# Performance work log

Hardware: AMD Instinct MI355X
Metric: run time of the kernel (lower is better)

The kernel has to match this reference:

```python
import jax, jax.numpy as jnp
import numpy as np

B, T, D, H = 8, 4096, 512, 64

def setup_inputs() -> dict:
    key = jax.random.key(0)
    ks = jax.random.split(key, 6)
    s = 0.02  # small init scale so exp(K), exp(wbias) stay numerically tame
    return {
        "x": jax.random.normal(ks[0], (B, T, D), dtype=jnp.float32),
        "wq": jax.random.normal(ks[1], (H, D), dtype=jnp.float32) * s,
        "bq": jnp.zeros((H,), dtype=jnp.float32),
        "wk": jax.random.normal(ks[2], (H, D), dtype=jnp.float32) * s,
        "bk": jnp.zeros((H,), dtype=jnp.float32),
        "wv": jax.random.normal(ks[3], (H, D), dtype=jnp.float32) * s,
        "bv": jnp.zeros((H,), dtype=jnp.float32),
        "wp": jax.random.normal(ks[4], (D, H), dtype=jnp.float32) * s,
        "bp": jnp.zeros((D,), dtype=jnp.float32),
        "wbias": jax.random.normal(ks[5], (T, T), dtype=jnp.float32) * s,
    }

def reference(x, wq, bq, wk, bk, wv, bv, wp, bp, wbias):
    # Q, K, V projections: [B, T, H]
    Q = jnp.einsum('btd,hd->bth', x, wq) + bq
    K = jnp.einsum('btd,hd->bth', x, wk) + bk
    V = jnp.einsum('btd,hd->bth', x, wv) + bv
    ew = jnp.exp(wbias)              # [T, T], computed once
    eK = jnp.exp(K)                  # [B, T, H]
    num = jnp.einsum('ts,bsh->bth', ew, eK * V)
    den = jnp.einsum('ts,bsh->bth', ew, eK)
    Yt = jax.nn.sigmoid(Q) * (num / den)
    # output projection back to dim: [B, T, D]
    return jnp.einsum('bth,dh->btd', Yt, wp) + bp
```

## Files before the change

kernel.cpp:

```cpp
#include <hip/hip_runtime.h>
#include <math.h>

typedef _Float16 f16;
typedef __attribute__((ext_vector_type(8))) _Float16 f16x8;
typedef __attribute__((ext_vector_type(4))) _Float16 f16x4;
typedef __attribute__((ext_vector_type(4))) float f32x4;
typedef __attribute__((ext_vector_type(16))) float f32x16;

#define MFMA16(a, b, c) __builtin_amdgcn_mfma_f32_16x16x32_f16((a), (b), (c), 0, 0, 0)
#define MFMA32(a, b, c) __builtin_amdgcn_mfma_f32_32x32x16_f16((a), (b), (c), 0, 0, 0)

__device__ __forceinline__ void gld16(const f16* g, f16* l) {
  __builtin_amdgcn_global_load_lds(
      (const __attribute__((address_space(1))) unsigned int*)g,
      (__attribute__((address_space(3))) unsigned int*)l, 16, 0, 0);
}

__device__ __forceinline__ f16x8 pack8(const float* src) {
  float4 f0 = *(const float4*)src;
  float4 f1 = *(const float4*)(src + 4);
  f16x8 v;
  v[0] = (f16)f0.x; v[1] = (f16)f0.y; v[2] = (f16)f0.z; v[3] = (f16)f0.w;
  v[4] = (f16)f1.x; v[5] = (f16)f1.y; v[6] = (f16)f1.z; v[7] = (f16)f1.w;
  return v;
}

__global__ __launch_bounds__(256) void prep_ewpw(const float* __restrict__ wb,
                                                 f16* __restrict__ ew,
                                                 const float* __restrict__ wq,
                                                 const float* __restrict__ wk,
                                                 const float* __restrict__ wv,
                                                 const float* __restrict__ wp,
                                                 f16* __restrict__ wqkvb,
                                                 f16* __restrict__ wpf) {
  const size_t stride = (size_t)gridDim.x * 256;
  const size_t total = (size_t)4096 * 4096 / 4;
  for (size_t i = (size_t)blockIdx.x * 256 + threadIdx.x; i < total; i += stride) {
    float4 f = ((const float4*)wb)[i];
    f16x4 o;
    o.x = (f16)expf(f.x); o.y = (f16)expf(f.y);
    o.z = (f16)expf(f.z); o.w = (f16)expf(f.w);
    ((f16x4*)ew)[i] = o;
  }
  if (blockIdx.x < 128) {
    int i = blockIdx.x * 256 + threadIdx.x;
    wqkvb[i] = (f16)wk[i];
    wqkvb[32768 + i] = (f16)wv[i];
    wqkvb[65536 + i] = (f16)wq[i];
  }
  if (blockIdx.x == 128) {
    const int tid = threadIdx.x;
#pragma unroll
    for (int u = 0; u < 16; ++u) {
      int d = u * 256 + tid;
      int dcb = d >> 8, c = (d >> 6) & 3, l = d & 63;
      const float* src = wp + (size_t)(dcb * 32 + (l & 31)) * 64 + c * 16 + (l >> 5) * 8;
      f16x8 o;
#pragma unroll
      for (int e = 0; e < 8; ++e) o[e] = (f16)src[e];
      *(f16x8*)(wpf + ((size_t)d << 3)) = o;
    }
  }
}

__global__ __launch_bounds__(256) void k1_qkv(const float* __restrict__ x,
                                              const f16* __restrict__ wqkvb,
                                              const float* __restrict__ bq,
                                              const float* __restrict__ bk,
                                              const float* __restrict__ bv,
                                              f16* __restrict__ sigQ,
                                              f16* __restrict__ XT) {
  __shared__ alignas(16) f16 sW[192 * 64];
  __shared__ alignas(16) f16 sX[64 * 64];
  const int tid = threadIdx.x;
  const int wave = tid >> 6, lane = tid & 63;
  const int m0 = blockIdx.x * 64;
  const int l15 = lane & 15;

  f32x4 accQ[4], accK[4], accV[4];
#pragma unroll
  for (int j = 0; j < 4; ++j) {
    accQ[j] = (f32x4){0.f, 0.f, 0.f, 0.f};
    accK[j] = (f32x4){0.f, 0.f, 0.f, 0.f};
    accV[j] = (f32x4){0.f, 0.f, 0.f, 0.f};
  }

  const int sc8 = tid & 7;
  const int wr8 = (tid >> 3) & 7;
  const int wcol = (sc8 ^ wr8) * 8;

  for (int ks = 0; ks < 512; ks += 64) {
#pragma unroll
    for (int q = 0; q < 6; ++q) {
      int r = q * 32 + (tid >> 3);
      gld16(wqkvb + (size_t)r * 512 + ks + wcol, &sW[r * 64 + sc8 * 8]);
    }
#pragma unroll
    for (int u = 0; u < 2; ++u) {
      int un = tid + u * 256;
      int r = un >> 3, c8 = un & 7;
      *(f16x8*)&sX[r * 64 + ((c8 ^ (r & 7)) * 8)] =
          pack8(x + (size_t)(m0 + r) * 512 + ks + c8 * 8);
    }
    __syncthreads();
#pragma unroll
    for (int kk = 0; kk < 2; ++kk) {
      const int c = kk * 4 + (lane >> 4);
      const int rK = wave * 16 + l15;
      const int rV = 64 + rK;
      f16x8 aK = *(const f16x8*)&sW[rK * 64 + ((c ^ (rK & 7)) * 8)];
      f16x8 aV = *(const f16x8*)&sW[rV * 64 + ((c ^ (rV & 7)) * 8)];
      f16x8 aQ = *(const f16x8*)&sX[rK * 64 + ((c ^ (rK & 7)) * 8)];
#pragma unroll
      for (int j = 0; j < 4; ++j) {
        const int rX = j * 16 + l15;
        const int rWq = 128 + j * 16 + l15;
        f16x8 bx = *(const f16x8*)&sX[rX * 64 + ((c ^ (rX & 7)) * 8)];
        f16x8 bw = *(const f16x8*)&sW[rWq * 64 + ((c ^ (rWq & 7)) * 8)];
        accK[j] = MFMA16(aK, bx, accK[j]);
        accV[j] = MFMA16(aV, bx, accV[j]);
        accQ[j] = MFMA16(aQ, bw, accQ[j]);
      }
    }
    __syncthreads();
  }
  const int b = m0 >> 12, t0 = m0 & 4095;
#pragma unroll
  for (int j = 0; j < 4; ++j) {
    const int h = j * 16 + l15;
    const float bqv = bq[h];
#pragma unroll
    for (int r = 0; r < 4; ++r) {
      const int m = m0 + wave * 16 + (lane >> 4) * 4 + r;
      const float v = accQ[j][r] + bqv;
      sigQ[(size_t)m * 64 + h] = (f16)(1.f / (1.f + expf(-v)));
    }
  }
#pragma unroll
  for (int r = 0; r < 4; ++r) {
    const int h = wave * 16 + (lane >> 4) * 4 + r;
    const float bkv = bk[h], bvv = bv[h];
    const size_t rowKV = (size_t)(b * 128 + h) * 4096;
    const size_t rowK = (size_t)(b * 128 + 64 + h) * 4096;
#pragma unroll
    for (int j = 0; j < 4; ++j) {
      const int t = t0 + j * 16 + l15;
      const float ek = expf(accK[j][r] + bkv);
      const float ev = accV[j][r] + bvv;
      XT[rowKV + t] = (f16)(ek * ev);
      XT[rowK + t] = (f16)ek;
    }
  }
}

__global__ __launch_bounds__(256) void k2_main(const f16* __restrict__ A,
                                               const f16* __restrict__ Bm,
                                               f16* __restrict__ P) {
  __shared__ alignas(16) f16 smem[2][2][8192];
  const int tid = threadIdx.x;
  const int w = tid >> 6, lane = tid & 63;
  const int wr = w >> 1, wc = w & 1;
  const int bid = blockIdx.x;
  const int x = bid & 7, y = bid >> 3;
  const int mt = x * 4 + (y >> 4);
  const int rem = y & 15;
  const int b = rem >> 1, kh = rem & 1;
  const int m0 = mt * 128;
  const size_t k0 = (size_t)kh * 2048;
  const f16* Ab = A + (size_t)m0 * 4096 + k0;
  const f16* Bb = Bm + (size_t)(b * 128) * 4096 + k0;

  int sRow[4], sCol[4];
#pragma unroll
  for (int u = 0; u < 4; ++u) {
    int d = u * 256 + tid;
    int p = d >> 4, c16 = d & 15;
    int oc = c16 ^ (p & 15);
    sRow[u] = p + 64 * (oc >> 3);
    sCol[u] = (oc & 7) * 8;
  }

  f32x16 accN[2], accD[2];
#pragma unroll
  for (int i = 0; i < 2; ++i)
#pragma unroll
    for (int r = 0; r < 16; ++r) { accN[i][r] = 0.f; accD[i][r] = 0.f; }

#define SB0 __builtin_amdgcn_sched_barrier(0)
#define K2_STAGE(buf, ks)                                                       \
  do {                                                                          \
    _Pragma("unroll") for (int u = 0; u < 4; ++u)                               \
        gld16(Ab + (size_t)sRow[u] * 4096 + (ks) + sCol[u],                     \
              &smem[buf][0][(u * 256 + tid) * 8]);                              \
    _Pragma("unroll") for (int u = 0; u < 4; ++u)                               \
        gld16(Bb + (size_t)sRow[u] * 4096 + (ks) + sCol[u],                     \
              &smem[buf][1][(u * 256 + tid) * 8]);                              \
  } while (0)

  K2_STAGE(0, 0);
  K2_STAGE(1, 64);
  asm volatile("s_waitcnt vmcnt(8)" ::: "memory");
  SB0;
  __builtin_amdgcn_s_barrier();
  SB0;

  const int l31 = lane & 31, l15 = lane & 15, lhi = lane >> 5;
  const int nk = 32;
  for (int t = 0; t < nk; ++t) {
    const int cur = t & 1;
    const f16* pA = smem[cur][0];
    const f16* pB = smem[cur][1];
    __builtin_amdgcn_s_setprio(1);
#pragma unroll
    for (int ks4 = 0; ks4 < 4; ++ks4) {
      const int kcc = ks4 * 2 + lhi;
      f16x8 a0 = *(const f16x8*)&pA[(l31)*128 + (((wr * 8 + kcc) ^ l15) * 8)];
      f16x8 a1 = *(const f16x8*)&pA[(32 + l31) * 128 + (((wr * 8 + kcc) ^ l15) * 8)];
      f16x8 bn = *(const f16x8*)&pB[(wc * 32 + l31) * 128 + ((kcc ^ l15) * 8)];
      f16x8 bd = *(const f16x8*)&pB[(wc * 32 + l31) * 128 + (((8 + kcc) ^ l15) * 8)];
      accN[0] = MFMA32(a0, bn, accN[0]);
      accD[0] = MFMA32(a0, bd, accD[0]);
      accN[1] = MFMA32(a1, bn, accN[1]);
      accD[1] = MFMA32(a1, bd, accD[1]);
    }
    __builtin_amdgcn_s_setprio(0);
    asm volatile("s_waitcnt lgkmcnt(0)" ::: "memory");
    SB0;
    __builtin_amdgcn_s_barrier();
    SB0;
    if (t + 2 < nk) {
      K2_STAGE(cur, (t + 2) * 64);
      asm volatile("s_waitcnt vmcnt(8)" ::: "memory");
    } else {
      asm volatile("s_waitcnt vmcnt(0)" ::: "memory");
    }
    SB0;
    __builtin_amdgcn_s_barrier();
    SB0;
  }
#undef K2_STAGE
#undef SB0

  f16* Pp = P + (size_t)kh * 4194304 + (size_t)(mt * 8 + b) * 16384;
#pragma unroll
  for (int i = 0; i < 2; ++i) {
#pragma unroll
    for (int r = 0; r < 16; ++r) {
      const int crow = wr * 64 + i * 32 + (r & 3) + 8 * (r >> 2) + 4 * lhi;
      Pp[crow * 128 + wc * 32 + l31] = (f16)accN[i][r];
      Pp[crow * 128 + 64 + wc * 32 + l31] = (f16)accD[i][r];
    }
  }
}

__global__ __launch_bounds__(256) void k2_red(const f16* __restrict__ P,
                                              const f16* __restrict__ sigQ,
                                              const f16* __restrict__ wpf,
                                              const float* __restrict__ bp,
                                              float* __restrict__ out) {
  __shared__ alignas(16) f16 sYt[128 * 72];
  const int tid = threadIdx.x;
  const int rid = blockIdx.x;
  const int mt = (rid & 7) * 4 + ((rid >> 3) & 3);
  const int b = rid >> 5;
  const int m0 = mt * 128;
  const f16* P0 = P + (size_t)(mt * 8 + b) * 16384;
  const f16* P1 = P0 + 4194304;

#pragma unroll
  for (int u = 0; u < 4; ++u) {
    const int e = u * 256 + tid;
    const int row = e >> 3, c = e & 7;
    f16x8 n0 = *(const f16x8*)(P0 + row * 128 + c * 8);
    f16x8 n1 = *(const f16x8*)(P1 + row * 128 + c * 8);
    f16x8 d0 = *(const f16x8*)(P0 + row * 128 + 64 + c * 8);
    f16x8 d1 = *(const f16x8*)(P1 + row * 128 + 64 + c * 8);
    f16x8 sq = *(const f16x8*)(sigQ + ((size_t)b * 4096 + m0 + row) * 64 + c * 8);
    f16x8 yv;
#pragma unroll
    for (int e8 = 0; e8 < 8; ++e8) {
      const float num = (float)n0[e8] + (float)n1[e8];
      const float den = (float)d0[e8] + (float)d1[e8];
      yv[e8] = (f16)((float)sq[e8] * num / den);
    }
    *(f16x8*)&sYt[row * 72 + c * 8] = yv;
  }
  __syncthreads();

  const int w = tid >> 6, lane = tid & 63;
  const int l31 = lane & 31, lhi = lane >> 5;
  f16x8 ay[4];
#pragma unroll
  for (int c = 0; c < 4; ++c)
    ay[c] = *(const f16x8*)&sYt[(w * 32 + l31) * 72 + c * 16 + lhi * 8];
#pragma unroll
  for (int cbo = 0; cbo < 16; ++cbo) {
    f32x16 oacc;
#pragma unroll
    for (int r = 0; r < 16; ++r) oacc[r] = 0.f;
#pragma unroll
    for (int c = 0; c < 4; ++c) {
      f16x8 bw = *(const f16x8*)(wpf + (((size_t)cbo * 4 + c) * 64 + lane) * 8);
      oacc = MFMA32(ay[c], bw, oacc);
    }
    const int od = cbo * 32 + l31;
    const float bpv = bp[od];
#pragma unroll
    for (int r = 0; r < 16; ++r) {
      const int orow = w * 32 + (r & 3) + 8 * (r >> 2) + 4 * lhi;
      out[((size_t)(b * 4096 + m0 + orow)) * 512 + od] = oacc[r] + bpv;
    }
  }
}

extern "C" void kernel_launch(void* const* d_in, const int* in_sizes, int n_in,
                              void* d_out, int out_size, void* d_ws, size_t ws_size,
                              hipStream_t stream) {
  const float* x = (const float*)d_in[0];
  const float* wq = (const float*)d_in[1];
  const float* bq = (const float*)d_in[2];
  const float* wk = (const float*)d_in[3];
  const float* bk = (const float*)d_in[4];
  const float* wv = (const float*)d_in[5];
  const float* bv = (const float*)d_in[6];
  const float* wp = (const float*)d_in[7];
  const float* bp = (const float*)d_in[8];
  const float* wbias = (const float*)d_in[9];
  float* out = (float*)d_out;

  char* ws = (char*)d_ws;
  f16* ew = (f16*)(ws);
  f16* XT = (f16*)(ws + 33554432);
  f16* sigQ = (f16*)(ws + 41943040);
  f16* P = (f16*)(ws + 46137344);
  f16* wqkvb = (f16*)(ws + 62914560);
  f16* wpf = (f16*)(ws + 63111168);

  prep_ewpw<<<4096, 256, 0, stream>>>(wbias, ew, wq, wk, wv, wp, wqkvb, wpf);
  k1_qkv<<<512, 256, 0, stream>>>(x, wqkvb, bq, bk, bv, sigQ, XT);
  k2_main<<<512, 256, 0, stream>>>(ew, XT, P);
  k2_red<<<256, 256, 0, stream>>>(P, sigQ, wpf, bp, out);
}
```

Baseline: 108.6 us.

## Fuse prep and QKV projection into one kernel; re-split reduction kernel

Merges the exp(wbias) prep kernel and the QKV projection kernel into a single launch. Blocks 0-511 do the projection and the remaining 2048 blocks do the exp conversion and the wp repack, so the two independent jobs run concurrently and one launch disappears. The projection now loads the fp32 weights and converts them to f16 inline instead of using a pre-converted f16 copy. That repeats the conversion work in every block and drops the async global-to-LDS load path. The reduction/output-projection kernel now uses 512 threads per block over half-row tiles with twice as many blocks, and each wave handles two output column blocks with two row groups.

Result: faster. 100.4 us (-7.5%).

```diff
diff --git a/kernel.cpp b/kernel.cpp
--- a/kernel.cpp
+++ b/kernel.cpp
@@ -25,54 +25,49 @@
   return v;
 }
 
-__global__ __launch_bounds__(256) void prep_ewpw(const float* __restrict__ wb,
-                                                 f16* __restrict__ ew,
-                                                 const float* __restrict__ wq,
-                                                 const float* __restrict__ wk,
-                                                 const float* __restrict__ wv,
-                                                 const float* __restrict__ wp,
-                                                 f16* __restrict__ wqkvb,
-                                                 f16* __restrict__ wpf) {
-  const size_t stride = (size_t)gridDim.x * 256;
-  const size_t total = (size_t)4096 * 4096 / 4;
-  for (size_t i = (size_t)blockIdx.x * 256 + threadIdx.x; i < total; i += stride) {
-    float4 f = ((const float4*)wb)[i];
-    f16x4 o;
-    o.x = (f16)expf(f.x); o.y = (f16)expf(f.y);
-    o.z = (f16)expf(f.z); o.w = (f16)expf(f.w);
-    ((f16x4*)ew)[i] = o;
-  }
-  if (blockIdx.x < 128) {
-    int i = blockIdx.x * 256 + threadIdx.x;
-    wqkvb[i] = (f16)wk[i];
-    wqkvb[32768 + i] = (f16)wv[i];
-    wqkvb[65536 + i] = (f16)wq[i];
-  }
-  if (blockIdx.x == 128) {
-    const int tid = threadIdx.x;
-#pragma unroll
-    for (int u = 0; u < 16; ++u) {
-      int d = u * 256 + tid;
-      int dcb = d >> 8, c = (d >> 6) & 3, l = d & 63;
-      const float* src = wp + (size_t)(dcb * 32 + (l & 31)) * 64 + c * 16 + (l >> 5) * 8;
-      f16x8 o;
-#pragma unroll
-      for (int e = 0; e < 8; ++e) o[e] = (f16)src[e];
-      *(f16x8*)(wpf + ((size_t)d << 3)) = o;
-    }
-  }
-}
-
-__global__ __launch_bounds__(256) void k1_qkv(const float* __restrict__ x,
-                                              const f16* __restrict__ wqkvb,
-                                              const float* __restrict__ bq,
-                                              const float* __restrict__ bk,
-                                              const float* __restrict__ bv,
-                                              f16* __restrict__ sigQ,
-                                              f16* __restrict__ XT) {
+__global__ __launch_bounds__(256) void k0(const float* __restrict__ x,
+                                          const float* __restrict__ wq,
+                                          const float* __restrict__ wk,
+                                          const float* __restrict__ wv,
+                                          const float* __restrict__ wp,
+                                          const float* __restrict__ bq,
+                                          const float* __restrict__ bk,
+                                          const float* __restrict__ bv,
+                                          const float* __restrict__ wbias,
+                                          f16* __restrict__ ew,
+                                          f16* __restrict__ wpf,
+                                          f16* __restrict__ sigQ,
+                                          f16* __restrict__ XT) {
   __shared__ alignas(16) f16 sW[192 * 64];
   __shared__ alignas(16) f16 sX[64 * 64];
   const int tid = threadIdx.x;
+
+  if (blockIdx.x >= 512) {
+    const int pb = blockIdx.x - 512;
+    const size_t stride = (size_t)(gridDim.x - 512) * 256;
+    const size_t total = (size_t)4096 * 4096 / 4;
+    for (size_t i = (size_t)pb * 256 + tid; i < total; i += stride) {
+      float4 f = ((const float4*)wbias)[i];
+      f16x4 o;
+      o.x = (f16)expf(f.x); o.y = (f16)expf(f.y);
+      o.z = (f16)expf(f.z); o.w = (f16)expf(f.w);
+      ((f16x4*)ew)[i] = o;
+    }
+    if (pb == 0) {
+#pragma unroll
+      for (int u = 0; u < 16; ++u) {
+        int d = u * 256 + tid;
+        int dcb = d >> 8, c = (d >> 6) & 3, l = d & 63;
+        const float* src = wp + (size_t)(dcb * 32 + (l & 31)) * 64 + c * 16 + (l >> 5) * 8;
+        f16x8 o;
+#pragma unroll
+        for (int e = 0; e < 8; ++e) o[e] = (f16)src[e];
+        *(f16x8*)(wpf + ((size_t)d << 3)) = o;
+      }
+    }
+    return;
+  }
+
   const int wave = tid >> 6, lane = tid & 63;
   const int m0 = blockIdx.x * 64;
   const int l15 = lane & 15;
@@ -85,15 +80,15 @@
     accV[j] = (f32x4){0.f, 0.f, 0.f, 0.f};
   }
 
-  const int sc8 = tid & 7;
-  const int wr8 = (tid >> 3) & 7;
-  const int wcol = (sc8 ^ wr8) * 8;
-
   for (int ks = 0; ks < 512; ks += 64) {
 #pragma unroll
-    for (int q = 0; q < 6; ++q) {
-      int r = q * 32 + (tid >> 3);
-      gld16(wqkvb + (size_t)r * 512 + ks + wcol, &sW[r * 64 + sc8 * 8]);
+    for (int u = 0; u < 6; ++u) {
+      int un = tid + u * 256;
+      int r = un >> 3, c8 = un & 7;
+      const float* src = (u < 2) ? (wk + (size_t)r * 512)
+                                 : (u < 4) ? (wv + (size_t)(r - 64) * 512)
+                                           : (wq + (size_t)(r - 128) * 512);
+      *(f16x8*)&sW[r * 64 + ((c8 ^ (r & 7)) * 8)] = pack8(src + ks + c8 * 8);
     }
 #pragma unroll
     for (int u = 0; u < 2; ++u) {
@@ -253,35 +248,36 @@
   }
 }
 
-__global__ __launch_bounds__(256) void k2_red(const f16* __restrict__ P,
+__global__ __launch_bounds__(512) void k2_red(const f16* __restrict__ P,
                                               const f16* __restrict__ sigQ,
                                               const f16* __restrict__ wpf,
                                               const float* __restrict__ bp,
                                               float* __restrict__ out) {
-  __shared__ alignas(16) f16 sYt[128 * 72];
+  __shared__ alignas(16) f16 sYt[64 * 72];
   const int tid = threadIdx.x;
   const int rid = blockIdx.x;
-  const int mt = (rid & 7) * 4 + ((rid >> 3) & 3);
-  const int b = rid >> 5;
+  const int xcd = rid & 7;
+  const int q = rid >> 3;
+  const int mt = xcd * 4 + (q & 3);
+  const int b = (q >> 2) & 7;
+  const int rh = q >> 5;
   const int m0 = mt * 128;
-  const f16* P0 = P + (size_t)(mt * 8 + b) * 16384;
+  const f16* P0 = P + (size_t)(mt * 8 + b) * 16384 + rh * 64 * 128;
   const f16* P1 = P0 + 4194304;
 
-#pragma unroll
-  for (int u = 0; u < 4; ++u) {
-    const int e = u * 256 + tid;
-    const int row = e >> 3, c = e & 7;
+  {
+    const int row = tid >> 3, c = tid & 7;
     f16x8 n0 = *(const f16x8*)(P0 + row * 128 + c * 8);
     f16x8 n1 = *(const f16x8*)(P1 + row * 128 + c * 8);
     f16x8 d0 = *(const f16x8*)(P0 + row * 128 + 64 + c * 8);
     f16x8 d1 = *(const f16x8*)(P1 + row * 128 + 64 + c * 8);
-    f16x8 sq = *(const f16x8*)(sigQ + ((size_t)b * 4096 + m0 + row) * 64 + c * 8);
+    f16x8 sq = *(const f16x8*)(sigQ + ((size_t)b * 4096 + m0 + rh * 64 + row) * 64 + c * 8);
     f16x8 yv;
 #pragma unroll
-    for (int e8 = 0; e8 < 8; ++e8) {
-      const float num = (float)n0[e8] + (float)n1[e8];
-      const float den = (float)d0[e8] + (float)d1[e8];
-      yv[e8] = (f16)((float)sq[e8] * num / den);
+    for (int e = 0; e < 8; ++e) {
+      const float num = (float)n0[e] + (float)n1[e];
+      const float den = (float)d0[e] + (float)d1[e];
+      yv[e] = (f16)((float)sq[e] * num / den);
     }
     *(f16x8*)&sYt[row * 72 + c * 8] = yv;
   }
@@ -289,26 +285,36 @@
 
   const int w = tid >> 6, lane = tid & 63;
   const int l31 = lane & 31, lhi = lane >> 5;
-  f16x8 ay[4];
-#pragma unroll
-  for (int c = 0; c < 4; ++c)
-    ay[c] = *(const f16x8*)&sYt[(w * 32 + l31) * 72 + c * 16 + lhi * 8];
-#pragma unroll
-  for (int cbo = 0; cbo < 16; ++cbo) {
-    f32x16 oacc;
-#pragma unroll
-    for (int r = 0; r < 16; ++r) oacc[r] = 0.f;
+  f16x8 ay[2][4];
+#pragma unroll
+  for (int rg = 0; rg < 2; ++rg)
+#pragma unroll
+    for (int c = 0; c < 4; ++c)
+      ay[rg][c] = *(const f16x8*)&sYt[(rg * 32 + l31) * 72 + c * 16 + lhi * 8];
+
+#pragma unroll
+  for (int c2 = 0; c2 < 2; ++c2) {
+    const int cbo = w * 2 + c2;
+    f32x16 oacc[2];
+#pragma unroll
+    for (int rg = 0; rg < 2; ++rg)
+#pragma unroll
+      for (int r = 0; r < 16; ++r) oacc[rg][r] = 0.f;
 #pragma unroll
     for (int c = 0; c < 4; ++c) {
       f16x8 bw = *(const f16x8*)(wpf + (((size_t)cbo * 4 + c) * 64 + lane) * 8);
-      oacc = MFMA32(ay[c], bw, oacc);
+      oacc[0] = MFMA32(ay[0][c], bw, oacc[0]);
+      oacc[1] = MFMA32(ay[1][c], bw, oacc[1]);
     }
     const int od = cbo * 32 + l31;
     const float bpv = bp[od];
 #pragma unroll
-    for (int r = 0; r < 16; ++r) {
-      const int orow = w * 32 + (r & 3) + 8 * (r >> 2) + 4 * lhi;
-      out[((size_t)(b * 4096 + m0 + orow)) * 512 + od] = oacc[r] + bpv;
+    for (int rg = 0; rg < 2; ++rg) {
+#pragma unroll
+      for (int r = 0; r < 16; ++r) {
+        const int orow = rh * 64 + rg * 32 + (r & 3) + 8 * (r >> 2) + 4 * lhi;
+        out[((size_t)(b * 4096 + m0 + orow)) * 512 + od] = oacc[rg][r] + bpv;
+      }
     }
   }
 }
@@ -333,11 +339,9 @@
   f16* XT = (f16*)(ws + 33554432);
   f16* sigQ = (f16*)(ws + 41943040);
   f16* P = (f16*)(ws + 46137344);
-  f16* wqkvb = (f16*)(ws + 62914560);
-  f16* wpf = (f16*)(ws + 63111168);
-
-  prep_ewpw<<<4096, 256, 0, stream>>>(wbias, ew, wq, wk, wv, wp, wqkvb, wpf);
-  k1_qkv<<<512, 256, 0, stream>>>(x, wqkvb, bq, bk, bv, sigQ, XT);
+  f16* wpf = (f16*)(ws + 62914560);
+
+  k0<<<2560, 256, 0, stream>>>(x, wq, wk, wv, wp, bq, bk, bv, wbias, ew, wpf, sigQ, XT);
   k2_main<<<512, 256, 0, stream>>>(ew, XT, P);
-  k2_red<<<256, 256, 0, stream>>>(P, sigQ, wpf, bp, out);
-}
+  k2_red<<<512, 512, 0, stream>>>(P, sigQ, wpf, bp, out);
+}
```
